# Performance work log

Measured on AMD Instinct MI355X. Metric: run time of the kernel, lower is better.

## Reference

```python
import jax, jax.numpy as jnp
import numpy as np

V, D, B, L = 433, 120, 4096, 16  # vocab, d_model, batch, seq_len
H4 = 4 * D
LN_EPS = 1e-5


def setup_inputs() -> dict:
    key = jax.random.key(0)
    ks = jax.random.split(key, 12)
    s = 1.0 / np.sqrt(D)  # PyTorch LSTM init range
    u = lambda k, shape: jax.random.uniform(k, shape, jnp.float32, -s, s)
    return {
        "x": jax.random.randint(ks[0], (B, L), 0, V, dtype=jnp.int32),
        "embed": jax.random.normal(ks[1], (V, D), jnp.float32) * 0.02,
        "Wih0": u(ks[2], (H4, D)), "Whh0": u(ks[3], (H4, D)),
        "bih0": u(ks[4], (H4,)), "bhh0": u(ks[5], (H4,)),
        "Wih1": u(ks[6], (H4, D)), "Whh1": u(ks[7], (H4, D)),
        "bih1": u(ks[8], (H4,)), "bhh1": u(ks[9], (H4,)),
        "gamma": jnp.ones((D,), jnp.float32),
        "beta": jnp.zeros((D,), jnp.float32),
    }


def _lstm_layer(x, Wih, Whh, bih, bhh):
    """One LSTM layer, batch_first input [B,L,D] -> [B,L,H]. PyTorch gate order i,f,g,o."""
    b, _, _ = x.shape
    h_dim = Whh.shape[1]
    # Precompute input contribution for all timesteps in one big GEMM.
    xg = jnp.einsum('bld,gd->blg', x, Wih) + bih + bhh  # [B,L,4H]

    def step(carry, g_t):
        h, c = carry
        gates = g_t + h @ Whh.T  # [B,4H]
        i, f, g, o = jnp.split(gates, 4, axis=-1)
        c = jax.nn.sigmoid(f) * c + jax.nn.sigmoid(i) * jnp.tanh(g)
        h = jax.nn.sigmoid(o) * jnp.tanh(c)
        return (h, c), h

    init = (jnp.zeros((b, h_dim), x.dtype), jnp.zeros((b, h_dim), x.dtype))
    _, hs = jax.lax.scan(step, init, jnp.swapaxes(xg, 0, 1))  # [L,B,H]
    return jnp.swapaxes(hs, 0, 1)


def _layernorm(h, gamma, beta):
    mu = jnp.mean(h, axis=-1, keepdims=True)
    var = jnp.mean(jnp.square(h - mu), axis=-1, keepdims=True)
    return (h - mu) / jnp.sqrt(var + LN_EPS) * gamma + beta


def reference(x, embed, Wih0, Whh0, bih0, bhh0, Wih1, Whh1, bih1, bhh1, gamma, beta):
    h = embed[x]                               # [B,L,D] token embedding
    h = _lstm_layer(h, Wih0, Whh0, bih0, bhh0)  # layer 0
    h = _lstm_layer(h, Wih1, Whh1, bih1, bhh1)  # layer 1
    out = _layernorm(h, gamma, beta)
    logits = jnp.einsum('bld,vd->blv', out, embed)  # tied-embedding head (no bias)
    return logits
```

## Files before the change

kernel.cpp:

```cpp
#include <hip/hip_runtime.h>


#define VSZ 433
#define DIM 120
#define BSZ 4096
#define SEQ 16
#define H4  480
#define MTOT (BSZ*SEQ)
#define KP  128
#define NPAD 448
#define NT_HEAD (NPAD/16)
#define TB  16
#define GP  484
#define HP  136

typedef unsigned int   u32;
typedef unsigned short u16;
typedef __attribute__((ext_vector_type(8))) short    v8bf;
typedef __attribute__((ext_vector_type(8))) _Float16 v8h;
typedef __attribute__((ext_vector_type(4))) float    v4f;

__device__ __forceinline__ float bf2f(u16 u){ union{u32 i;float f;}z; z.i=((u32)u)<<16; return z.f; }
__device__ __forceinline__ u16 f2bf(float f){
  union{float f;u32 u;}z; z.f=f;
  u32 u = z.u + 0x7fffu + ((z.u>>16)&1u);
  return (u16)(u>>16);
}
__device__ __forceinline__ u32 packh2(float a, float b){
  union{_Float16 h[2]; u32 u;} z;
  z.h[0] = (_Float16)a; z.h[1] = (_Float16)b;
  return z.u;
}

#define EW_OFF   0u
#define B1S_OFF  831488u
#define EMBP_OFF 833408u
#define HB0_OFF  948096u

__global__ __launch_bounds__(512) void k_ew(const float* __restrict__ embed,
                                            const float* __restrict__ Wih0,
                                            const float* __restrict__ bih0,
                                            const float* __restrict__ bhh0,
                                            float* __restrict__ EW)
{
  __shared__ float e[DIM];
  const int v = blockIdx.x, tid = threadIdx.x;
  if (tid < DIM) e[tid] = embed[v*DIM + tid];
  __syncthreads();
  if (tid < H4) {
    float acc = bih0[tid] + bhh0[tid];
    #pragma unroll
    for (int k0 = 0; k0 < DIM; k0 += 4) {
      float4 w = *(const float4*)(Wih0 + tid*DIM + k0);
      acc = fmaf(e[k0+0], w.x, acc);
      acc = fmaf(e[k0+1], w.y, acc);
      acc = fmaf(e[k0+2], w.z, acc);
      acc = fmaf(e[k0+3], w.w, acc);
    }
    EW[v*H4 + tid] = acc;
  }
}

__global__ __launch_bounds__(256) void k_prep2(const float* __restrict__ embed,
                                               const float* __restrict__ bih1,
                                               const float* __restrict__ bhh1,
                                               u16* __restrict__ embP,
                                               float* __restrict__ b1s)
{
  const int idx = blockIdx.x*256 + threadIdx.x;
  if (idx < NPAD*KP) {
    int n = idx >> 7, k = idx & 127;
    embP[idx] = (n < VSZ && k < DIM) ? f2bf(embed[n*DIM + k]) : (u16)0;
  } else if (idx < NPAD*KP + H4) {
    int g = idx - NPAD*KP;
    b1s[g] = bih1[g] + bhh1[g];
  }
}

__global__ __launch_bounds__(512) void k_rec0(const float* __restrict__ Whh,
                                              const float* __restrict__ EW,
                                              const int* __restrict__ x,
                                              _Float16* __restrict__ hb0)
{
  __shared__ float gLs[TB][GP];
  __shared__ __align__(16) _Float16 hLh[TB][HP];
  __shared__ int xL[TB*SEQ];

  const int tid  = threadIdx.x;
  const int wave = tid >> 6, lane = tid & 63;
  const int cl   = lane & 15, quad = lane >> 4;
  const int b0   = blockIdx.x * TB;

  for (int i = tid; i < TB*SEQ; i += 512) xL[i] = x[b0*SEQ + i];
  for (int i = tid; i < TB*HP; i += 512) (&hLh[0][0])[i] = (_Float16)0.f;
  __syncthreads();

  v8h Bf[4][4];
  #pragma unroll
  for (int i = 0; i < 4; ++i) {
    const int nt = wave*4 + i;
    const bool vld = (nt < 30);
    const int n = vld ? nt*16 + cl : 0;
    #pragma unroll
    for (int kt = 0; kt < 4; ++kt) {
      const int k0 = kt*32 + quad*8;
      v8h f = {0,0,0,0,0,0,0,0};
      if (vld && k0 < DIM) {
        float4 q0 = *(const float4*)(Whh + n*DIM + k0);
        float4 q1 = *(const float4*)(Whh + n*DIM + k0 + 4);
        f[0]=(_Float16)q0.x; f[1]=(_Float16)q0.y; f[2]=(_Float16)q0.z; f[3]=(_Float16)q0.w;
        f[4]=(_Float16)q1.x; f[5]=(_Float16)q1.y; f[6]=(_Float16)q1.z; f[7]=(_Float16)q1.w;
      }
      Bf[i][kt] = f;
    }
  }

  float srcv[4][4];
  auto load_src = [&](int t) {
    #pragma unroll
    for (int i = 0; i < 4; ++i) {
      const int nt = wave*4 + i;
      if (nt < 30) {
        const int n = nt*16 + cl;
        #pragma unroll
        for (int r = 0; r < 4; ++r)
          srcv[i][r] = EW[(size_t)xL[(quad*4 + r)*SEQ + t]*H4 + n];
      }
    }
  };
  load_src(0);

  const int prow = wave*2;
  const bool act = lane < 60;
  const int d0   = lane*2;
  float C[2][2] = {{0.f,0.f},{0.f,0.f}};

  for (int t = 0; t < SEQ; ++t) {
    __syncthreads();
    v8h Af[4];
    #pragma unroll
    for (int kt = 0; kt < 4; ++kt)
      Af[kt] = *(const v8h*)&hLh[cl][kt*32 + quad*8];
    v4f acc[4];
    #pragma unroll
    for (int i = 0; i < 4; ++i) {
      acc[i][0]=srcv[i][0]; acc[i][1]=srcv[i][1];
      acc[i][2]=srcv[i][2]; acc[i][3]=srcv[i][3];
    }
    #pragma unroll
    for (int i = 0; i < 4; ++i)
      if (wave*4 + i < 30) {
        #pragma unroll
        for (int kt = 0; kt < 4; ++kt)
          acc[i] = __builtin_amdgcn_mfma_f32_16x16x32_f16(Af[kt], Bf[i][kt], acc[i], 0, 0, 0);
      }
    if (t + 1 < SEQ) load_src(t + 1);
    #pragma unroll
    for (int i = 0; i < 4; ++i) {
      const int nt = wave*4 + i;
      if (nt < 30) {
        #pragma unroll
        for (int r = 0; r < 4; ++r)
          gLs[quad*4 + r][nt*16 + cl] = acc[i][r];
      }
    }
    __syncthreads();
    #pragma unroll
    for (int rr = 0; rr < 2; ++rr) {
      const int row = prow + rr;
      if (act) {
        const float2 gi = *(const float2*)&gLs[row][d0      ];
        const float2 gf = *(const float2*)&gLs[row][d0 + 120];
        const float2 gg = *(const float2*)&gLs[row][d0 + 240];
        const float2 go = *(const float2*)&gLs[row][d0 + 360];
        float h2[2];
        #pragma unroll
        for (int k = 0; k < 2; ++k) {
          const float vi = k ? gi.y : gi.x, vf = k ? gf.y : gf.x;
          const float vg = k ? gg.y : gg.x, vo = k ? go.y : go.x;
          const float si = 1.f / (1.f + __expf(-vi));
          const float sf = 1.f / (1.f + __expf(-vf));
          const float tg = 1.f - 2.f / (__expf(2.f*vg) + 1.f);
          const float so = 1.f / (1.f + __expf(-vo));
          const float c  = sf * C[rr][k] + si * tg;
          C[rr][k] = c;
          const float tc = 1.f - 2.f / (__expf(2.f*c) + 1.f);
          h2[k] = so * tc;
        }
        *(u32*)&hLh[row][d0] = packh2(h2[0], h2[1]);
        *(u32*)&hb0[((size_t)t*BSZ + b0 + row)*KP + d0] = packh2(h2[0], h2[1]);
      } else {
        *(u32*)&hb0[((size_t)t*BSZ + b0 + row)*KP + 120 + 2*(lane - 60)] = 0u;
      }
    }
  }
}

__global__ __launch_bounds__(512) void k_rec1(const float* __restrict__ Wih1,
                                              const float* __restrict__ Whh1,
                                              const float* __restrict__ b1s,
                                              const _Float16* __restrict__ hb0,
                                              const float* __restrict__ gamma,
                                              const float* __restrict__ beta,
                                              const u16* __restrict__ embP,
                                              float* __restrict__ out)
{
  __shared__ float gLs[TB][GP];
  __shared__ __align__(16) _Float16 hLh[TB][HP];
  __shared__ __align__(16) u16 hnL[TB][HP];
  __shared__ __align__(16) u16 embL[NPAD][HP];

  const int tid  = threadIdx.x;
  const int wave = tid >> 6, lane = tid & 63;
  const int cl   = lane & 15, quad = lane >> 4;
  const int b0   = blockIdx.x * TB;

  for (int i = tid; i < TB*HP; i += 512) (&hLh[0][0])[i] = (_Float16)0.f;
  for (int c = tid; c < NPAD*16; c += 512) {
    const int rw = c >> 4, c16 = c & 15;
    *(v8bf*)&embL[rw][c16*8] = *(const v8bf*)&embP[(size_t)rw*KP + c16*8];
  }

  v8h Bi[4][4], Bh[4][4];
  float bias[4];
  #pragma unroll
  for (int i = 0; i < 4; ++i) {
    const int nt = wave*4 + i;
    const bool vld = (nt < 30);
    const int n = vld ? nt*16 + cl : 0;
    bias[i] = vld ? b1s[n] : 0.f;
    #pragma unroll
    for (int kt = 0; kt < 4; ++kt) {
      const int k0 = kt*32 + quad*8;
      v8h fi = {0,0,0,0,0,0,0,0}, fh = {0,0,0,0,0,0,0,0};
      if (vld && k0 < DIM) {
        float4 q0 = *(const float4*)(Wih1 + n*DIM + k0);
        float4 q1 = *(const float4*)(Wih1 + n*DIM + k0 + 4);
        fi[0]=(_Float16)q0.x; fi[1]=(_Float16)q0.y; fi[2]=(_Float16)q0.z; fi[3]=(_Float16)q0.w;
        fi[4]=(_Float16)q1.x; fi[5]=(_Float16)q1.y; fi[6]=(_Float16)q1.z; fi[7]=(_Float16)q1.w;
        float4 p0 = *(const float4*)(Whh1 + n*DIM + k0);
        float4 p1 = *(const float4*)(Whh1 + n*DIM + k0 + 4);
        fh[0]=(_Float16)p0.x; fh[1]=(_Float16)p0.y; fh[2]=(_Float16)p0.z; fh[3]=(_Float16)p0.w;
        fh[4]=(_Float16)p1.x; fh[5]=(_Float16)p1.y; fh[6]=(_Float16)p1.z; fh[7]=(_Float16)p1.w;
      }
      Bi[i][kt] = fi;
      Bh[i][kt] = fh;
    }
  }

  const int prow = wave*2;
  const bool act = lane < 60;
  const int d0   = lane*2;
  float gmm[2] = {0.f, 0.f}, bta[2] = {0.f, 0.f};
  if (act) {
    gmm[0] = gamma[d0]; gmm[1] = gamma[d0+1];
    bta[0] = beta[d0];  bta[1] = beta[d0+1];
  }
  float C[2][2] = {{0.f,0.f},{0.f,0.f}};

  v8h A0n[4];
  #pragma unroll
  for (int kt = 0; kt < 4; ++kt)
    A0n[kt] = *(const v8h*)&hb0[((size_t)0*BSZ + b0 + cl)*KP + kt*32 + quad*8];
  __syncthreads();

  for (int t = 0; t < SEQ; ++t) {
    v8h A0c[4], A1[4];
    #pragma unroll
    for (int kt = 0; kt < 4; ++kt) A0c[kt] = A0n[kt];
    #pragma unroll
    for (int kt = 0; kt < 4; ++kt)
      A1[kt] = *(const v8h*)&hLh[cl][kt*32 + quad*8];
    if (t + 1 < SEQ) {
      #pragma unroll
      for (int kt = 0; kt < 4; ++kt)
        A0n[kt] = *(const v8h*)&hb0[((size_t)(t+1)*BSZ + b0 + cl)*KP + kt*32 + quad*8];
    }
    v4f acc[4];
    #pragma unroll
    for (int i = 0; i < 4; ++i)
      acc[i] = (v4f){bias[i], bias[i], bias[i], bias[i]};
    #pragma unroll
    for (int i = 0; i < 4; ++i)
      if (wave*4 + i < 30) {
        #pragma unroll
        for (int kt = 0; kt < 4; ++kt) {
          acc[i] = __builtin_amdgcn_mfma_f32_16x16x32_f16(A0c[kt], Bi[i][kt], acc[i], 0, 0, 0);
          acc[i] = __builtin_amdgcn_mfma_f32_16x16x32_f16(A1[kt],  Bh[i][kt], acc[i], 0, 0, 0);
        }
      }
    #pragma unroll
    for (int i = 0; i < 4; ++i) {
      const int nt = wave*4 + i;
      if (nt < 30) {
        #pragma unroll
        for (int r = 0; r < 4; ++r)
          gLs[quad*4 + r][nt*16 + cl] = acc[i][r];
      }
    }
    __syncthreads();
    float h2[2][2] = {{0.f,0.f},{0.f,0.f}};
    float s1[2] = {0.f, 0.f}, s2[2] = {0.f, 0.f};
    #pragma unroll
    for (int rr = 0; rr < 2; ++rr) {
      const int row = prow + rr;
      if (act) {
        const float2 gi = *(const float2*)&gLs[row][d0      ];
        const float2 gf = *(const float2*)&gLs[row][d0 + 120];
        const float2 gg = *(const float2*)&gLs[row][d0 + 240];
        const float2 go = *(const float2*)&gLs[row][d0 + 360];
        #pragma unroll
        for (int k = 0; k < 2; ++k) {
          const float vi = k ? gi.y : gi.x, vf = k ? gf.y : gf.x;
          const float vg = k ? gg.y : gg.x, vo = k ? go.y : go.x;
          const float si = 1.f / (1.f + __expf(-vi));
          const float sf = 1.f / (1.f + __expf(-vf));
          const float tg = 1.f - 2.f / (__expf(2.f*vg) + 1.f);
          const float so = 1.f / (1.f + __expf(-vo));
          const float c  = sf * C[rr][k] + si * tg;
          C[rr][k] = c;
          const float tc = 1.f - 2.f / (__expf(2.f*c) + 1.f);
          const float h  = so * tc;
          h2[rr][k] = h;
          s1[rr] += h;
          s2[rr] = fmaf(h, h, s2[rr]);
        }
        *(u32*)&hLh[row][d0] = packh2(h2[rr][0], h2[rr][1]);
      }
    }
    #pragma unroll
    for (int m = 32; m >= 1; m >>= 1) {
      s1[0] += __shfl_xor(s1[0], m);
      s2[0] += __shfl_xor(s2[0], m);
      s1[1] += __shfl_xor(s1[1], m);
      s2[1] += __shfl_xor(s2[1], m);
    }
    #pragma unroll
    for (int rr = 0; rr < 2; ++rr) {
      const int row = prow + rr;
      const float mu = s1[rr] * (1.f/DIM);
      const float var = s2[rr] * (1.f/DIM) - mu*mu;
      const float rs = rsqrtf(var + 1e-5f);
      if (act) {
        const float v0 = fmaf((h2[rr][0] - mu)*rs, gmm[0], bta[0]);
        const float v1 = fmaf((h2[rr][1] - mu)*rs, gmm[1], bta[1]);
        *(u32*)&hnL[row][d0] = (u32)f2bf(v0) | ((u32)f2bf(v1) << 16);
      } else {
        *(u32*)&hnL[row][120 + 2*(lane - 60)] = 0u;
      }
    }
    __syncthreads();

    {
      v8bf a[4];
      #pragma unroll
      for (int kt = 0; kt < 4; ++kt)
        a[kt] = *(const v8bf*)&hnL[cl][kt*32 + quad*8];
      #pragma unroll
      for (int j = 0; j < 4; ++j) {
        const int nt = wave + 8*j;
        if (nt < NT_HEAD) {
          const int n = nt*16 + cl;
          v8bf bfr[4];
          #pragma unroll
          for (int kt = 0; kt < 4; ++kt)
            bfr[kt] = *(const v8bf*)&embL[n][kt*32 + quad*8];
          v4f hacc = {0.f, 0.f, 0.f, 0.f};
          #pragma unroll
          for (int kt = 0; kt < 4; ++kt)
            hacc = __builtin_amdgcn_mfma_f32_16x16x32_bf16(a[kt], bfr[kt], hacc, 0, 0, 0);
          if (n < VSZ) {
            #pragma unroll
            for (int r = 0; r < 4; ++r)
              out[((size_t)(b0 + quad*4 + r)*SEQ + t)*VSZ + n] = hacc[r];
          }
        }
      }
    }
  }
}

extern "C" void kernel_launch(void* const* d_in, const int* in_sizes, int n_in,
                              void* d_out, int out_size, void* d_ws, size_t ws_size,
                              hipStream_t stream)
{
  (void)in_sizes; (void)n_in; (void)out_size; (void)ws_size;
  const int*   x     = (const int*)d_in[0];
  const float* embed = (const float*)d_in[1];
  const float* Wih0  = (const float*)d_in[2];
  const float* Whh0  = (const float*)d_in[3];
  const float* bih0  = (const float*)d_in[4];
  const float* bhh0  = (const float*)d_in[5];
  const float* Wih1  = (const float*)d_in[6];
  const float* Whh1  = (const float*)d_in[7];
  const float* bih1  = (const float*)d_in[8];
  const float* bhh1  = (const float*)d_in[9];
  const float* gamma = (const float*)d_in[10];
  const float* beta  = (const float*)d_in[11];

  char* ws = (char*)d_ws;
  float*     EW   = (float*)(ws + EW_OFF);
  float*     b1s  = (float*)(ws + B1S_OFF);
  u16*       embP = (u16*)(ws + EMBP_OFF);
  _Float16*  hb0  = (_Float16*)(ws + HB0_OFF);

  k_ew   <<<VSZ, 512, 0, stream>>>(embed, Wih0, bih0, bhh0, EW);
  k_prep2<<<226, 256, 0, stream>>>(embed, bih1, bhh1, embP, b1s);
  k_rec0 <<<BSZ/TB, 512, 0, stream>>>(Whh0, EW, x, hb0);
  k_rec1 <<<BSZ/TB, 512, 0, stream>>>(Wih1, Whh1, b1s, hb0, gamma, beta, embP, (float*)d_out);
}
```

Baseline: 258.3 us.

## Fuse both LSTM layer kernels and merge prep kernels into one launch

New measurement: 257.2 us. About the same (-0.4%).

```diff
diff --git a/kernel.cpp b/kernel.cpp
--- a/kernel.cpp
+++ b/kernel.cpp
@@ -6,7 +6,6 @@
 #define BSZ 4096
 #define SEQ 16
 #define H4  480
-#define MTOT (BSZ*SEQ)
 #define KP  128
 #define NPAD 448
 #define NT_HEAD (NPAD/16)
@@ -20,7 +19,6 @@
 typedef __attribute__((ext_vector_type(8))) _Float16 v8h;
 typedef __attribute__((ext_vector_type(4))) float    v4f;
 
-__device__ __forceinline__ float bf2f(u16 u){ union{u32 i;float f;}z; z.i=((u32)u)<<16; return z.f; }
 __device__ __forceinline__ u16 f2bf(float f){
   union{float f;u32 u;}z; z.f=f;
   u32 u = z.u + 0x7fffu + ((z.u>>16)&1u);
@@ -37,189 +35,190 @@
 #define EMBP_OFF 833408u
 #define HB0_OFF  948096u
 
-__global__ __launch_bounds__(512) void k_ew(const float* __restrict__ embed,
-                                            const float* __restrict__ Wih0,
-                                            const float* __restrict__ bih0,
-                                            const float* __restrict__ bhh0,
-                                            float* __restrict__ EW)
+#define PREP_BLKS 113
+
+__global__ __launch_bounds__(512) void k_init(const float* __restrict__ embed,
+                                              const float* __restrict__ Wih0,
+                                              const float* __restrict__ bih0,
+                                              const float* __restrict__ bhh0,
+                                              const float* __restrict__ bih1,
+                                              const float* __restrict__ bhh1,
+                                              float* __restrict__ EW,
+                                              u16* __restrict__ embP,
+                                              float* __restrict__ b1s)
 {
   __shared__ float e[DIM];
-  const int v = blockIdx.x, tid = threadIdx.x;
-  if (tid < DIM) e[tid] = embed[v*DIM + tid];
-  __syncthreads();
-  if (tid < H4) {
-    float acc = bih0[tid] + bhh0[tid];
-    #pragma unroll
-    for (int k0 = 0; k0 < DIM; k0 += 4) {
-      float4 w = *(const float4*)(Wih0 + tid*DIM + k0);
-      acc = fmaf(e[k0+0], w.x, acc);
-      acc = fmaf(e[k0+1], w.y, acc);
-      acc = fmaf(e[k0+2], w.z, acc);
-      acc = fmaf(e[k0+3], w.w, acc);
-    }
-    EW[v*H4 + tid] = acc;
+  const int tid = threadIdx.x;
+  if (blockIdx.x < VSZ) {
+    const int v = blockIdx.x;
+    if (tid < DIM) e[tid] = embed[v*DIM + tid];
+    __syncthreads();
+    if (tid < H4) {
+      float acc = bih0[tid] + bhh0[tid];
+      #pragma unroll
+      for (int k0 = 0; k0 < DIM; k0 += 4) {
+        float4 w = *(const float4*)(Wih0 + tid*DIM + k0);
+        acc = fmaf(e[k0+0], w.x, acc);
+        acc = fmaf(e[k0+1], w.y, acc);
+        acc = fmaf(e[k0+2], w.z, acc);
+        acc = fmaf(e[k0+3], w.w, acc);
+      }
+      EW[v*H4 + tid] = acc;
+    }
+  } else {
+    const int idx = (blockIdx.x - VSZ)*512 + tid;
+    if (idx < NPAD*KP) {
+      int n = idx >> 7, k = idx & 127;
+      embP[idx] = (n < VSZ && k < DIM) ? f2bf(embed[n*DIM + k]) : (u16)0;
+    } else if (idx < NPAD*KP + H4) {
+      int g = idx - NPAD*KP;
+      b1s[g] = bih1[g] + bhh1[g];
+    }
   }
 }
 
-__global__ __launch_bounds__(256) void k_prep2(const float* __restrict__ embed,
-                                               const float* __restrict__ bih1,
-                                               const float* __restrict__ bhh1,
-                                               u16* __restrict__ embP,
-                                               float* __restrict__ b1s)
-{
-  const int idx = blockIdx.x*256 + threadIdx.x;
-  if (idx < NPAD*KP) {
-    int n = idx >> 7, k = idx & 127;
-    embP[idx] = (n < VSZ && k < DIM) ? f2bf(embed[n*DIM + k]) : (u16)0;
-  } else if (idx < NPAD*KP + H4) {
-    int g = idx - NPAD*KP;
-    b1s[g] = bih1[g] + bhh1[g];
-  }
-}
-
-__global__ __launch_bounds__(512) void k_rec0(const float* __restrict__ Whh,
-                                              const float* __restrict__ EW,
-                                              const int* __restrict__ x,
-                                              _Float16* __restrict__ hb0)
-{
-  __shared__ float gLs[TB][GP];
-  __shared__ __align__(16) _Float16 hLh[TB][HP];
-  __shared__ int xL[TB*SEQ];
-
-  const int tid  = threadIdx.x;
-  const int wave = tid >> 6, lane = tid & 63;
-  const int cl   = lane & 15, quad = lane >> 4;
-  const int b0   = blockIdx.x * TB;
-
-  for (int i = tid; i < TB*SEQ; i += 512) xL[i] = x[b0*SEQ + i];
-  for (int i = tid; i < TB*HP; i += 512) (&hLh[0][0])[i] = (_Float16)0.f;
-  __syncthreads();
-
-  v8h Bf[4][4];
-  #pragma unroll
-  for (int i = 0; i < 4; ++i) {
-    const int nt = wave*4 + i;
-    const bool vld = (nt < 30);
-    const int n = vld ? nt*16 + cl : 0;
-    #pragma unroll
-    for (int kt = 0; kt < 4; ++kt) {
-      const int k0 = kt*32 + quad*8;
-      v8h f = {0,0,0,0,0,0,0,0};
-      if (vld && k0 < DIM) {
-        float4 q0 = *(const float4*)(Whh + n*DIM + k0);
-        float4 q1 = *(const float4*)(Whh + n*DIM + k0 + 4);
-        f[0]=(_Float16)q0.x; f[1]=(_Float16)q0.y; f[2]=(_Float16)q0.z; f[3]=(_Float16)q0.w;
-        f[4]=(_Float16)q1.x; f[5]=(_Float16)q1.y; f[6]=(_Float16)q1.z; f[7]=(_Float16)q1.w;
-      }
-      Bf[i][kt] = f;
-    }
-  }
-
-  float srcv[4][4];
-  auto load_src = [&](int t) {
-    #pragma unroll
-    for (int i = 0; i < 4; ++i) {
-      const int nt = wave*4 + i;
-      if (nt < 30) {
-        const int n = nt*16 + cl;
-        #pragma unroll
-        for (int r = 0; r < 4; ++r)
-          srcv[i][r] = EW[(size_t)xL[(quad*4 + r)*SEQ + t]*H4 + n];
-      }
-    }
-  };
-  load_src(0);
-
-  const int prow = wave*2;
-  const bool act = lane < 60;
-  const int d0   = lane*2;
-  float C[2][2] = {{0.f,0.f},{0.f,0.f}};
-
-  for (int t = 0; t < SEQ; ++t) {
-    __syncthreads();
-    v8h Af[4];
-    #pragma unroll
-    for (int kt = 0; kt < 4; ++kt)
-      Af[kt] = *(const v8h*)&hLh[cl][kt*32 + quad*8];
-    v4f acc[4];
-    #pragma unroll
-    for (int i = 0; i < 4; ++i) {
-      acc[i][0]=srcv[i][0]; acc[i][1]=srcv[i][1];
-      acc[i][2]=srcv[i][2]; acc[i][3]=srcv[i][3];
-    }
-    #pragma unroll
-    for (int i = 0; i < 4; ++i)
-      if (wave*4 + i < 30) {
-        #pragma unroll
-        for (int kt = 0; kt < 4; ++kt)
-          acc[i] = __builtin_amdgcn_mfma_f32_16x16x32_f16(Af[kt], Bf[i][kt], acc[i], 0, 0, 0);
-      }
-    if (t + 1 < SEQ) load_src(t + 1);
-    #pragma unroll
-    for (int i = 0; i < 4; ++i) {
-      const int nt = wave*4 + i;
-      if (nt < 30) {
-        #pragma unroll
-        for (int r = 0; r < 4; ++r)
-          gLs[quad*4 + r][nt*16 + cl] = acc[i][r];
-      }
-    }
-    __syncthreads();
-    #pragma unroll
-    for (int rr = 0; rr < 2; ++rr) {
-      const int row = prow + rr;
-      if (act) {
-        const float2 gi = *(const float2*)&gLs[row][d0      ];
-        const float2 gf = *(const float2*)&gLs[row][d0 + 120];
-        const float2 gg = *(const float2*)&gLs[row][d0 + 240];
-        const float2 go = *(const float2*)&gLs[row][d0 + 360];
-        float h2[2];
-        #pragma unroll
-        for (int k = 0; k < 2; ++k) {
-          const float vi = k ? gi.y : gi.x, vf = k ? gf.y : gf.x;
-          const float vg = k ? gg.y : gg.x, vo = k ? go.y : go.x;
-          const float si = 1.f / (1.f + __expf(-vi));
-          const float sf = 1.f / (1.f + __expf(-vf));
-          const float tg = 1.f - 2.f / (__expf(2.f*vg) + 1.f);
-          const float so = 1.f / (1.f + __expf(-vo));
-          const float c  = sf * C[rr][k] + si * tg;
-          C[rr][k] = c;
-          const float tc = 1.f - 2.f / (__expf(2.f*c) + 1.f);
-          h2[k] = so * tc;
-        }
-        *(u32*)&hLh[row][d0] = packh2(h2[0], h2[1]);
-        *(u32*)&hb0[((size_t)t*BSZ + b0 + row)*KP + d0] = packh2(h2[0], h2[1]);
-      } else {
-        *(u32*)&hb0[((size_t)t*BSZ + b0 + row)*KP + 120 + 2*(lane - 60)] = 0u;
-      }
-    }
-  }
-}
-
-__global__ __launch_bounds__(512) void k_rec1(const float* __restrict__ Wih1,
-                                              const float* __restrict__ Whh1,
-                                              const float* __restrict__ b1s,
-                                              const _Float16* __restrict__ hb0,
-                                              const float* __restrict__ gamma,
-                                              const float* __restrict__ beta,
-                                              const u16* __restrict__ embP,
-                                              float* __restrict__ out)
+__global__ __launch_bounds__(512) void k_rec(const float* __restrict__ Whh0,
+                                             const float* __restrict__ EW,
+                                             const int* __restrict__ x,
+                                             const float* __restrict__ Wih1,
+                                             const float* __restrict__ Whh1,
+                                             const float* __restrict__ b1s,
+                                             const float* __restrict__ gamma,
+                                             const float* __restrict__ beta,
+                                             const u16* __restrict__ embP,
+                                             _Float16* __restrict__ hb0,
+                                             float* __restrict__ out)
 {
   __shared__ float gLs[TB][GP];
   __shared__ __align__(16) _Float16 hLh[TB][HP];
   __shared__ __align__(16) u16 hnL[TB][HP];
   __shared__ __align__(16) u16 embL[NPAD][HP];
+  __shared__ int xL[TB*SEQ];
 
   const int tid  = threadIdx.x;
   const int wave = tid >> 6, lane = tid & 63;
   const int cl   = lane & 15, quad = lane >> 4;
   const int b0   = blockIdx.x * TB;
 
+  for (int i = tid; i < TB*SEQ; i += 512) xL[i] = x[b0*SEQ + i];
   for (int i = tid; i < TB*HP; i += 512) (&hLh[0][0])[i] = (_Float16)0.f;
   for (int c = tid; c < NPAD*16; c += 512) {
     const int rw = c >> 4, c16 = c & 15;
     *(v8bf*)&embL[rw][c16*8] = *(const v8bf*)&embP[(size_t)rw*KP + c16*8];
   }
+  __syncthreads();
+
+  const int prow = wave*2;
+  const bool act = lane < 60;
+  const int d0   = lane*2;
+
+  {
+    v8h Bf[4][4];
+    #pragma unroll
+    for (int i = 0; i < 4; ++i) {
+      const int nt = wave*4 + i;
+      const bool vld = (nt < 30);
+      const int n = vld ? nt*16 + cl : 0;
+      #pragma unroll
+      for (int kt = 0; kt < 4; ++kt) {
+        const int k0 = kt*32 + quad*8;
+        v8h f = {0,0,0,0,0,0,0,0};
+        if (vld && k0 < DIM) {
+          float4 q0 = *(const float4*)(Whh0 + n*DIM + k0);
+          float4 q1 = *(const float4*)(Whh0 + n*DIM + k0 + 4);
+          f[0]=(_Float16)q0.x; f[1]=(_Float16)q0.y; f[2]=(_Float16)q0.z; f[3]=(_Float16)q0.w;
+          f[4]=(_Float16)q1.x; f[5]=(_Float16)q1.y; f[6]=(_Float16)q1.z; f[7]=(_Float16)q1.w;
+        }
+        Bf[i][kt] = f;
+      }
+    }
+
+    float srcv[4][4];
+    auto load_src = [&](int t) {
+      #pragma unroll
+      for (int i = 0; i < 4; ++i) {
+        const int nt = wave*4 + i;
+        if (nt < 30) {
+          const int n = nt*16 + cl;
+          #pragma unroll
+          for (int r = 0; r < 4; ++r)
+            srcv[i][r] = EW[(size_t)xL[(quad*4 + r)*SEQ + t]*H4 + n];
+        }
+      }
+    };
+    load_src(0);
+
+    float C0[2][2] = {{0.f,0.f},{0.f,0.f}};
+
+    for (int t = 0; t < SEQ; ++t) {
+      __syncthreads();
+      v8h Af[4];
+      #pragma unroll
+      for (int kt = 0; kt < 4; ++kt)
+        Af[kt] = *(const v8h*)&hLh[cl][kt*32 + quad*8];
+      v4f acc[4];
+      #pragma unroll
+      for (int i = 0; i < 4; ++i) {
+        acc[i][0]=srcv[i][0]; acc[i][1]=srcv[i][1];
+        acc[i][2]=srcv[i][2]; acc[i][3]=srcv[i][3];
+      }
+      #pragma unroll
+      for (int i = 0; i < 4; ++i)
+        if (wave*4 + i < 30) {
+          #pragma unroll
+          for (int kt = 0; kt < 4; ++kt)
+            acc[i] = __builtin_amdgcn_mfma_f32_16x16x32_f16(Af[kt], Bf[i][kt], acc[i], 0, 0, 0);
+        }
+      if (t + 1 < SEQ) load_src(t + 1);
+      #pragma unroll
+      for (int i = 0; i < 4; ++i) {
+        const int nt = wave*4 + i;
+        if (nt < 30) {
+          #pragma unroll
+          for (int r = 0; r < 4; ++r)
+            gLs[quad*4 + r][nt*16 + cl] = acc[i][r];
+        }
+      }
+      __syncthreads();
+      #pragma unroll
+      for (int rr = 0; rr < 2; ++rr) {
+        const int row = prow + rr;
+        if (act) {
+          const float2 gi = *(const float2*)&gLs[row][d0      ];
+          const float2 gf = *(const float2*)&gLs[row][d0 + 120];
+          const float2 gg = *(const float2*)&gLs[row][d0 + 240];
+          const float2 go = *(const float2*)&gLs[row][d0 + 360];
+          float h2[2];
+          #pragma unroll
+          for (int k = 0; k < 2; ++k) {
+            const float vi = k ? gi.y : gi.x, vf = k ? gf.y : gf.x;
+            const float vg = k ? gg.y : gg.x, vo = k ? go.y : go.x;
+            const float si = 1.f / (1.f + __expf(-vi));
+            const float sf = 1.f / (1.f + __expf(-vf));
+            const float tg = 1.f - 2.f / (__expf(2.f*vg) + 1.f);
+            const float so = 1.f / (1.f + __expf(-vo));
+            const float c  = sf * C0[rr][k] + si * tg;
+            C0[rr][k] = c;
+            const float tc = 1.f - 2.f / (__expf(2.f*c) + 1.f);
+            h2[k] = so * tc;
+          }
+          *(u32*)&hLh[row][d0] = packh2(h2[0], h2[1]);
+          *(u32*)&hb0[((size_t)t*BSZ + b0 + row)*KP + d0] = packh2(h2[0], h2[1]);
+        } else {
+          *(u32*)&hb0[((size_t)t*BSZ + b0 + row)*KP + 120 + 2*(lane - 60)] = 0u;
+        }
+      }
+    }
+  }
+
+  __syncthreads();
+
+  const float* Wih1p = Wih1;
+  const float* Whh1p = Whh1;
+  const float* b1sp  = b1s;
+  asm volatile("" : "+s"(Wih1p), "+s"(Whh1p), "+s"(b1sp) :: "memory");
+
+  for (int i = tid; i < TB*HP; i += 512) (&hLh[0][0])[i] = (_Float16)0.f;
 
   v8h Bi[4][4], Bh[4][4];
   float bias[4];
@@ -228,18 +227,18 @@
     const int nt = wave*4 + i;
     const bool vld = (nt < 30);
     const int n = vld ? nt*16 + cl : 0;
-    bias[i] = vld ? b1s[n] : 0.f;
+    bias[i] = vld ? b1sp[n] : 0.f;
     #pragma unroll
     for (int kt = 0; kt < 4; ++kt) {
       const int k0 = kt*32 + quad*8;
       v8h fi = {0,0,0,0,0,0,0,0}, fh = {0,0,0,0,0,0,0,0};
       if (vld && k0 < DIM) {
-        float4 q0 = *(const float4*)(Wih1 + n*DIM + k0);
-        float4 q1 = *(const float4*)(Wih1 + n*DIM + k0 + 4);
+        float4 q0 = *(const float4*)(Wih1p + n*DIM + k0);
+        float4 q1 = *(const float4*)(Wih1p + n*DIM + k0 + 4);
         fi[0]=(_Float16)q0.x; fi[1]=(_Float16)q0.y; fi[2]=(_Float16)q0.z; fi[3]=(_Float16)q0.w;
         fi[4]=(_Float16)q1.x; fi[5]=(_Float16)q1.y; fi[6]=(_Float16)q1.z; fi[7]=(_Float16)q1.w;
-        float4 p0 = *(const float4*)(Whh1 + n*DIM + k0);
-        float4 p1 = *(const float4*)(Whh1 + n*DIM + k0 + 4);
+        float4 p0 = *(const float4*)(Whh1p + n*DIM + k0);
+        float4 p1 = *(const float4*)(Whh1p + n*DIM + k0 + 4);
         fh[0]=(_Float16)p0.x; fh[1]=(_Float16)p0.y; fh[2]=(_Float16)p0.z; fh[3]=(_Float16)p0.w;
         fh[4]=(_Float16)p1.x; fh[5]=(_Float16)p1.y; fh[6]=(_Float16)p1.z; fh[7]=(_Float16)p1.w;
       }
@@ -248,15 +247,12 @@
     }
   }
 
-  const int prow = wave*2;
-  const bool act = lane < 60;
-  const int d0   = lane*2;
   float gmm[2] = {0.f, 0.f}, bta[2] = {0.f, 0.f};
   if (act) {
     gmm[0] = gamma[d0]; gmm[1] = gamma[d0+1];
     bta[0] = beta[d0];  bta[1] = beta[d0+1];
   }
-  float C[2][2] = {{0.f,0.f},{0.f,0.f}};
+  float C1[2][2] = {{0.f,0.f},{0.f,0.f}};
 
   v8h A0n[4];
   #pragma unroll
@@ -317,8 +313,8 @@
           const float sf = 1.f / (1.f + __expf(-vf));
           const float tg = 1.f - 2.f / (__expf(2.f*vg) + 1.f);
           const float so = 1.f / (1.f + __expf(-vo));
-          const float c  = sf * C[rr][k] + si * tg;
-          C[rr][k] = c;
+          const float c  = sf * C1[rr][k] + si * tg;
+          C1[rr][k] = c;
           const float tc = 1.f - 2.f / (__expf(2.f*c) + 1.f);
           const float h  = so * tc;
           h2[rr][k] = h;
@@ -404,8 +400,8 @@
   u16*       embP = (u16*)(ws + EMBP_OFF);
   _Float16*  hb0  = (_Float16*)(ws + HB0_OFF);
 
-  k_ew   <<<VSZ, 512, 0, stream>>>(embed, Wih0, bih0, bhh0, EW);
-  k_prep2<<<226, 256, 0, stream>>>(embed, bih1, bhh1, embP, b1s);
-  k_rec0 <<<BSZ/TB, 512, 0, stream>>>(Whh0, EW, x, hb0);
-  k_rec1 <<<BSZ/TB, 512, 0, stream>>>(Wih1, Whh1, b1s, hb0, gamma, beta, embP, (float*)d_out);
+  k_init<<<VSZ + PREP_BLKS, 512, 0, stream>>>(embed, Wih0, bih0, bhh0, bih1, bhh1,
+                                              EW, embP, b1s);
+  k_rec <<<BSZ/TB, 512, 0, stream>>>(Whh0, EW, x, Wih1, Whh1, b1s, gamma, beta,
+                                     embP, hb0, (float*)d_out);
 }
```
